# Kernel optimization log

Hardware: AMD Instinct MI355X
Metric: run time of the kernel (lower is better)

The kernel has to match this reference:

```python
import jax, jax.numpy as jnp
import numpy as np
import math

DIM = 147      # input feature dim
EMB = 64       # in_dim * head_cnt
M = 32         # int(EMB * kernel_ratio)
EPS_LN = 1e-5
EPS = 1e-8


def layer_norm(x, g, b, eps=EPS_LN):
    mu = jnp.mean(x, axis=-1, keepdims=True)
    var = jnp.mean(jnp.square(x - mu), axis=-1, keepdims=True)
    return (x - mu) * jax.lax.rsqrt(var + eps) * g + b


def prm_exp(x, W_rf):
    # x: [b, t, e], W_rf: [m, e]
    xd = 0.5 * jnp.sum(x * x, axis=-1, keepdims=True)        # [b, t, 1]
    wtx = jnp.einsum('bte,me->btm', x, W_rf)                  # [b, t, m]
    return jnp.exp(wtx - xd) / math.sqrt(M)


def setup_inputs() -> dict:
    key = jax.random.key(0)
    ks = jax.random.split(key, 16)
    B, T = 32, 3136
    s_in = 1.0 / math.sqrt(DIM)
    s_emb = 1.0 / math.sqrt(EMB)
    inp = {
        'x':      jax.random.normal(ks[0], (B, T, DIM), jnp.float32),
        'w_kqv':  jax.random.uniform(ks[1], (3 * EMB, DIM), jnp.float32, -s_in, s_in),
        'b_kqv':  jax.random.uniform(ks[2], (3 * EMB,), jnp.float32, -s_in, s_in),
        'w_proj': jax.random.uniform(ks[3], (EMB, EMB), jnp.float32, -s_emb, s_emb),
        'b_proj': jax.random.uniform(ks[4], (EMB,), jnp.float32, -s_emb, s_emb),
        'g1':     jnp.ones((DIM,), jnp.float32),
        'beta1':  jnp.zeros((DIM,), jnp.float32),
        'g2':     jnp.ones((EMB,), jnp.float32),
        'beta2':  jnp.zeros((EMB,), jnp.float32),
        'w_m1':   jax.random.uniform(ks[5], (EMB, EMB), jnp.float32, -s_emb, s_emb),
        'b_m1':   jax.random.uniform(ks[6], (EMB,), jnp.float32, -s_emb, s_emb),
        'w_m2':   jax.random.uniform(ks[7], (EMB, EMB), jnp.float32, -s_emb, s_emb),
        'b_m2':   jax.random.uniform(ks[8], (EMB,), jnp.float32, -s_emb, s_emb),
        # orthogonal random-feature matrix scaled by sqrt(m) (buffer 'w')
        'W_rf':   jnp.asarray(np.linalg.qr(np.random.RandomState(0).randn(EMB, EMB))[0][:M] * math.sqrt(M), jnp.float32),
    }
    return inp


def reference(x, w_kqv, b_kqv, w_proj, b_proj, g1, beta1, g2, beta2,
              w_m1, b_m1, w_m2, b_m2, W_rf):
    # --- single_attn(norm1(x)) ---
    xn = layer_norm(x, g1, beta1)
    kqv = xn @ w_kqv.T + b_kqv                                  # [b, t, 3e]
    k, q, v = jnp.split(kqv, 3, axis=-1)
    kp = prm_exp(k, W_rf)                                       # [b, t, m]
    qp = prm_exp(q, W_rf)                                       # [b, t, m]
    D = jnp.einsum('btm,bm->bt', qp, kp.sum(axis=1))[..., None]  # [b, t, 1]
    kptv = jnp.einsum('bte,btm->bem', v, kp)                    # [b, e, m]
    y = jnp.einsum('btm,bem->bte', qp, kptv) / (D + EPS)        # [b, t, e]
    y = v + (y @ w_proj.T + b_proj)                             # residual on v
    # --- y + mlp(norm2(y)) ---
    yn = layer_norm(y, g2, beta2)
    h = jax.nn.gelu(yn @ w_m1.T + b_m1, approximate=False)
    out = y + (h @ w_m2.T + b_m2)
    return out
```

## Files before the change

kernel.cpp:

```cpp
#include <hip/hip_runtime.h>
#include <hip/hip_bf16.h>

#define BB 32
#define TT 3136
#define DD 147
#define EE 64
#define MM 32
#define BT (BB*TT)

typedef __hip_bfloat16 bf16;
typedef __attribute__((ext_vector_type(8))) short s8v;
typedef __attribute__((ext_vector_type(4))) float f4v;

__device__ __forceinline__ float b2f(bf16 v){ return __bfloat162float(v); }
__device__ __forceinline__ bf16 f2b(float v){ return __float2bfloat16(v); }
__device__ __forceinline__ unsigned pack2(float a, float b){
  union { bf16 h[2]; unsigned u; } cv; cv.h[0]=f2b(a); cv.h[1]=f2b(b); return cv.u;
}

template<typename T>
__device__ __forceinline__ float cvt1(T v);
template<> __device__ __forceinline__ float cvt1<float>(float v){ return v; }
template<> __device__ __forceinline__ float cvt1<bf16>(bf16 v){ return __bfloat162float(v); }

__global__ void k_detect(const unsigned* __restrict__ g1u, int* __restrict__ flagp){
  if (threadIdx.x == 0 && blockIdx.x == 0)
    *flagp = (g1u[0] == 0x3F803F80u) ? 1 : 0;
}

template<typename T>
__device__ void cvt_body(int idx,
    const T* wkqv, const T* bkqv, const T* Wrf, const T* wproj, const T* bproj,
    const T* g2, const T* be2, const T* wm1, const T* bm1, const T* wm2,
    const T* bm2, const T* g1, const T* be1,
    bf16* Bprep, bf16* WrfB, bf16* w0B, float* bprojF,
    float* g2F, float* be2F, bf16* w1B, float* bm1F, bf16* w2B,
    float* bm2F, float* c2F)
{
  if (idx < 30720){
    int n = idx/160, k = idx - n*160;
    Bprep[idx] = f2b(k < DD ? cvt1(wkqv[n*DD + k]) * cvt1(g1[k]) : 0.f);
    return;
  }
  idx -= 30720;
  if (idx < 2048){ WrfB[idx] = f2b(cvt1(Wrf[idx])); return; }
  idx -= 2048;
  if (idx < 4608){
    int e = idx/72, c = idx - e*72;
    w0B[idx] = f2b(c < 64 ? cvt1(wproj[e*64 + c]) : 0.f); return;
  }
  idx -= 4608;
  if (idx < 64){ bprojF[idx] = cvt1(bproj[idx]); return; }
  idx -= 64;
  if (idx < 64){ g2F[idx] = cvt1(g2[idx]); return; }
  idx -= 64;
  if (idx < 64){ be2F[idx] = cvt1(be2[idx]); return; }
  idx -= 64;
  if (idx < 4608){
    int e = idx/72, c = idx - e*72;
    w1B[idx] = f2b(c < 64 ? cvt1(wm1[e*64 + c]) : 0.f); return;
  }
  idx -= 4608;
  if (idx < 64){ bm1F[idx] = cvt1(bm1[idx]); return; }
  idx -= 64;
  if (idx < 4608){
    int e = idx/72, c = idx - e*72;
    w2B[idx] = f2b(c < 64 ? cvt1(wm2[e*64 + c]) : 0.f); return;
  }
  idx -= 4608;
  if (idx < 64){ bm2F[idx] = cvt1(bm2[idx]); return; }
  idx -= 64;
  if (idx < 192){
    float s = cvt1(bkqv[idx]);
    for (int k=0; k<DD; ++k)
      s = fmaf(cvt1(wkqv[idx*DD + k]), cvt1(be1[k]), s);
    c2F[idx] = s; return;
  }
}

__global__ void k_cvt(const void* wkqv, const void* bkqv, const void* Wrf,
    const void* wproj, const void* bproj, const void* g2, const void* be2,
    const void* wm1, const void* bm1, const void* wm2, const void* bm2,
    const void* g1, const void* be1, const int* __restrict__ flagp,
    bf16* Bprep, bf16* WrfB, bf16* w0B, float* bprojF,
    float* g2F, float* be2F, bf16* w1B, float* bm1F, bf16* w2B,
    float* bm2F, float* c2F,
    float* __restrict__ kptvF, float* __restrict__ ksumF)
{
  int idx = blockIdx.x*256 + threadIdx.x;
  if (idx < 65536) kptvF[idx] = 0.f;
  if (idx < 1024)  ksumF[idx] = 0.f;
  if (*flagp)
    cvt_body<bf16>(idx, (const bf16*)wkqv, (const bf16*)bkqv, (const bf16*)Wrf,
      (const bf16*)wproj, (const bf16*)bproj, (const bf16*)g2, (const bf16*)be2,
      (const bf16*)wm1, (const bf16*)bm1, (const bf16*)wm2, (const bf16*)bm2,
      (const bf16*)g1, (const bf16*)be1,
      Bprep, WrfB, w0B, bprojF, g2F, be2F, w1B, bm1F, w2B, bm2F, c2F);
  else
    cvt_body<float>(idx, (const float*)wkqv, (const float*)bkqv, (const float*)Wrf,
      (const float*)wproj, (const float*)bproj, (const float*)g2, (const float*)be2,
      (const float*)wm1, (const float*)bm1, (const float*)wm2, (const float*)bm2,
      (const float*)g1, (const float*)be1,
      Bprep, WrfB, w0B, bprojF, g2F, be2F, w1B, bm1F, w2B, bm2F, c2F);
}

__global__ __launch_bounds__(256) void k_a2(
    const void* __restrict__ x, const int* __restrict__ flagp,
    const bf16* __restrict__ Bprep, const float* __restrict__ c2F,
    const bf16* __restrict__ WrfB,
    bf16* __restrict__ qp, bf16* __restrict__ v,
    float* __restrict__ kptvF, float* __restrict__ ksumF)
{
  __shared__ __align__(16) char smem[40320];
  bf16* xRaw = (bf16*)smem;
  bf16* aS   = (bf16*)(smem + 18816);
  bf16* vT   = (bf16*)(smem + 18816);
  bf16* kpT  = (bf16*)(smem + 18816 + 9216);

  int tid = threadIdx.x;
  size_t t0 = (size_t)blockIdx.x*64;
  int b = blockIdx.x / 49;

  int tw = tid>>6, lane = tid&63, quad = lane>>4, r = lane&15;
  int tRow = tw*16 + quad*4;

  if (*flagp){
    const uint4* xg = (const uint4*)((const bf16*)x + t0*DD);
    uint4* xo = (uint4*)xRaw;
    for (int c=tid; c<1176; c+=256) xo[c] = xg[c];
  } else {
    const float4* xg = (const float4*)((const float*)x + t0*DD);
    uint2* xo = (uint2*)xRaw;
    for (int c=tid; c<2352; c+=256){
      float4 f = xg[c];
      uint2 u; u.x = pack2(f.x, f.y); u.y = pack2(f.z, f.w);
      xo[c] = u;
    }
  }
  __syncthreads();

  int ti = lane>>2, s = lane&3;
  int row = tw*16 + ti;
  const bf16* srow = xRaw + row*DD;
  float s1 = 0.f, s2 = 0.f;
  #pragma unroll
  for (int j=0; j<37; ++j){
    int e = s + 4*j;
    if (e < DD){
      float vx = b2f(srow[e]);
      s1 += vx;
      s2 = fmaf(vx, vx, s2);
    }
  }
  s1 += __shfl_xor(s1,1); s1 += __shfl_xor(s1,2);
  s2 += __shfl_xor(s2,1); s2 += __shfl_xor(s2,2);
  float mu  = s1 * (1.f/147.f);
  float var = s2 * (1.f/147.f) - mu*mu;
  float rn  = rsqrtf(var + 1e-5f);

  bf16* arow = aS + row*168;
  #pragma unroll
  for (int j=0; j<37; ++j){
    int e = s + 4*j;
    arow[e] = (e < DD) ? f2b((b2f(srow[e]) - mu)*rn) : f2b(0.f);
  }
  arow[148+s] = f2b(0.f); arow[152+s] = f2b(0.f); arow[156+s] = f2b(0.f);

  f4v zero = {0.f,0.f,0.f,0.f};

  f4v acc[12];
  #pragma unroll
  for (int nt=0; nt<12; ++nt) acc[nt] = zero;
  const bf16* aBase = &aS[(tw*16+r)*168 + quad*8];
  const bf16* bBase = &Bprep[r*160 + quad*8];
  #pragma unroll 1
  for (int ks=0; ks<5; ++ks){
    s8v a = *((const s8v*)(aBase + ks*32));
    #pragma unroll
    for (int nt=0; nt<12; ++nt){
      s8v bw = *((const s8v*)(bBase + nt*16*160 + ks*32));
      acc[nt] = __builtin_amdgcn_mfma_f32_16x16x32_bf16(a, bw, acc[nt], 0,0,0);
    }
  }

  float c2v[12];
  #pragma unroll
  for (int nt=0; nt<12; ++nt) c2v[nt] = c2F[nt*16 + r];

  float vv[4][4];
  #pragma unroll
  for (int nt=8; nt<12; ++nt){
    #pragma unroll
    for (int reg=0; reg<4; ++reg){
      vv[nt-8][reg] = acc[nt][reg] + c2v[nt];
      v[(t0 + tRow + reg)*64 + (nt-8)*16 + r] = f2b(vv[nt-8][reg]);
    }
  }

  float kq[8][4];
  #pragma unroll
  for (int nt=0; nt<8; ++nt)
    #pragma unroll
    for (int reg=0; reg<4; ++reg)
      kq[nt][reg] = acc[nt][reg] + c2v[nt];

  bf16* kqW = (bf16*)(smem + tw*4704);
  #pragma unroll
  for (int nt=0; nt<8; ++nt)
    #pragma unroll
    for (int reg=0; reg<4; ++reg)
      kqW[(quad*4+reg)*136 + nt*16 + r] = f2b(kq[nt][reg]);

  float xdk[4], xdq[4];
  #pragma unroll
  for (int reg=0; reg<4; ++reg){
    float sk = 0.f, sq = 0.f;
    #pragma unroll
    for (int nt=0; nt<4; ++nt){
      sk = fmaf(kq[nt][reg],   kq[nt][reg],   sk);
      sq = fmaf(kq[nt+4][reg], kq[nt+4][reg], sq);
    }
    #pragma unroll
    for (int off=1; off<16; off<<=1){
      sk += __shfl_xor(sk, off);
      sq += __shfl_xor(sq, off);
    }
    xdk[reg] = 0.5f*sk;
    xdq[reg] = 0.5f*sq;
  }

  f4v accP[2] = {zero, zero}, accQ[2] = {zero, zero};
  #pragma unroll
  for (int ks=0; ks<2; ++ks){
    s8v ak = *((const s8v*)&kqW[r*136 + ks*32 + quad*8]);
    s8v aq = *((const s8v*)&kqW[r*136 + 64 + ks*32 + quad*8]);
    #pragma unroll
    for (int nt=0; nt<2; ++nt){
      s8v wf = *((const s8v*)&WrfB[(nt*16+r)*64 + ks*32 + quad*8]);
      accP[nt] = __builtin_amdgcn_mfma_f32_16x16x32_bf16(ak, wf, accP[nt], 0,0,0);
      accQ[nt] = __builtin_amdgcn_mfma_f32_16x16x32_bf16(aq, wf, accQ[nt], 0,0,0);
    }
  }
  float kpv[2][4];
  #pragma unroll
  for (int nt=0; nt<2; ++nt){
    #pragma unroll
    for (int reg=0; reg<4; ++reg){
      size_t gt = t0 + tRow + reg;
      kpv[nt][reg] = expf(accP[nt][reg] - xdk[reg]) * 0.17677669529663687f;
      qp[gt*32 + nt*16 + r] = f2b(expf(accQ[nt][reg] - xdq[reg]) * 0.17677669529663687f);
    }
  }
  __syncthreads();

  #pragma unroll
  for (int nt=0; nt<4; ++nt){
    *((unsigned*)&vT[(nt*16+r)*72 + tRow])     = pack2(vv[nt][0], vv[nt][1]);
    *((unsigned*)&vT[(nt*16+r)*72 + tRow + 2]) = pack2(vv[nt][2], vv[nt][3]);
  }
  #pragma unroll
  for (int nt=0; nt<2; ++nt){
    *((unsigned*)&kpT[(nt*16+r)*72 + tRow])     = pack2(kpv[nt][0], kpv[nt][1]);
    *((unsigned*)&kpT[(nt*16+r)*72 + tRow + 2]) = pack2(kpv[nt][2], kpv[nt][3]);
  }

  float ks0 = kpv[0][0]+kpv[0][1]+kpv[0][2]+kpv[0][3];
  float ks1 = kpv[1][0]+kpv[1][1]+kpv[1][2]+kpv[1][3];
  ks0 += __shfl_xor(ks0, 16); ks0 += __shfl_xor(ks0, 32);
  ks1 += __shfl_xor(ks1, 16); ks1 += __shfl_xor(ks1, 32);
  if (lane < 16){
    atomicAdd(&ksumF[b*32 + r],      ks0);
    atomicAdd(&ksumF[b*32 + 16 + r], ks1);
  }
  __syncthreads();

  f4v accKV[2] = {zero, zero};
  #pragma unroll
  for (int kh=0; kh<2; ++kh){
    s8v av = *((const s8v*)&vT[(tw*16+r)*72 + kh*32 + quad*8]);
    #pragma unroll
    for (int nt=0; nt<2; ++nt){
      s8v bk = *((const s8v*)&kpT[(nt*16+r)*72 + kh*32 + quad*8]);
      accKV[nt] = __builtin_amdgcn_mfma_f32_16x16x32_bf16(av, bk, accKV[nt], 0,0,0);
    }
  }
  float* dst = kptvF + b*2048;
  #pragma unroll
  for (int nt=0; nt<2; ++nt)
    #pragma unroll
    for (int reg=0; reg<4; ++reg)
      atomicAdd(&dst[(tw*16 + quad*4 + reg)*32 + nt*16 + r], accKV[nt][reg]);
}

__global__ __launch_bounds__(256,2) void k_b(
    const bf16* __restrict__ qp, const bf16* __restrict__ v,
    const float* __restrict__ kptvF, const float* __restrict__ ksumF,
    const bf16* __restrict__ w0B, const float* __restrict__ bprojF,
    const float* __restrict__ g2F, const float* __restrict__ be2F,
    const bf16* __restrict__ w1B, const float* __restrict__ bm1F,
    const bf16* __restrict__ w2B, const float* __restrict__ bm2F,
    const int* __restrict__ flagp, void* __restrict__ outp)
{
  __shared__ __align__(16) bf16 qpS[64*40];
  __shared__ __align__(16) bf16 kvS[64*40];
  __shared__ __align__(16) bf16 w0S[64*72];
  __shared__ __align__(16) bf16 w1S[64*72];
  __shared__ __align__(16) bf16 w2S[64*72];
  __shared__ __align__(16) bf16 vS[64*72];
  __shared__ __align__(16) bf16 stA[64*72];
  __shared__ __align__(16) bf16 stB[64*72];
  __shared__ float ksS[32];
  __shared__ float bpS[64], b1S[64], b2S[64], gS[64], btS[64];

  int flag = *flagp;
  int tid = threadIdx.x;
  int b = blockIdx.y;
  int gt0 = b*TT + blockIdx.x*64;

  {
    int t = tid>>2, q = tid&3;
    uint4 u = ((const uint4*)(qp + (size_t)gt0*32))[tid];
    *((uint4*)&qpS[t*40 + q*8]) = u;
  }
  for (int i=tid; i<512; i+=256){
    int e = i>>3, q = i&7;
    float4 f = ((const float4*)(kptvF + b*2048))[i];
    union { bf16 h[4]; uint2 u; } cv;
    cv.h[0]=f2b(f.x); cv.h[1]=f2b(f.y); cv.h[2]=f2b(f.z); cv.h[3]=f2b(f.w);
    *((uint2*)&kvS[e*40 + q*4]) = cv.u;
  }
  for (int i=tid; i<512; i+=256){
    int t = i>>3, q = i&7;
    uint4 u = ((const uint4*)(v + (size_t)gt0*64))[i];
    *((uint4*)&vS[t*72 + q*8]) = u;
  }
  for (int i=tid; i<576; i+=256) ((uint4*)w0S)[i] = ((const uint4*)w0B)[i];
  for (int i=tid; i<576; i+=256) ((uint4*)w1S)[i] = ((const uint4*)w1B)[i];
  for (int i=tid; i<576; i+=256) ((uint4*)w2S)[i] = ((const uint4*)w2B)[i];
  if (tid<32) ksS[tid] = ksumF[b*32+tid];
  if (tid<64){
    bpS[tid]=bprojF[tid]; b1S[tid]=bm1F[tid]; b2S[tid]=bm2F[tid];
    gS[tid]=g2F[tid]; btS[tid]=be2F[tid];
  }
  __syncthreads();

  int tw = tid>>6, lane = tid&63, quad = lane>>4, r = lane&15;
  int tRow = tw*16 + quad*4;
  f4v zero = {0.f,0.f,0.f,0.f};

  float dpart;
  {
    int ti = lane>>2, sl = lane&3;
    const bf16* qrow = &qpS[(tw*16+ti)*40];
    float s = 0.f;
    #pragma unroll
    for (int m=0; m<8; ++m) s = fmaf(b2f(qrow[sl*8+m]), ksS[sl*8+m], s);
    s += __shfl_xor(s,1); s += __shfl_xor(s,2);
    dpart = s;
  }
  float Dinv[4];
  #pragma unroll
  for (int reg=0; reg<4; ++reg){
    float d = __shfl(dpart, (lane & 0x30) + 4*reg);
    Dinv[reg] = 1.f/(d + 1e-8f);
  }

  f4v accA[4];
  {
    s8v aq = *((const s8v*)&qpS[(tw*16+r)*40 + quad*8]);
    #pragma unroll
    for (int nt=0; nt<4; ++nt){
      s8v bk = *((const s8v*)&kvS[(nt*16+r)*40 + quad*8]);
      accA[nt] = __builtin_amdgcn_mfma_f32_16x16x32_bf16(aq, bk, zero, 0,0,0);
    }
  }

  #pragma unroll
  for (int nt=0; nt<4; ++nt)
    #pragma unroll
    for (int reg=0; reg<4; ++reg)
      stA[(tRow+reg)*72 + nt*16 + r] = f2b(accA[nt][reg]*Dinv[reg]);

  f4v accY[4] = {zero, zero, zero, zero};
  #pragma unroll
  for (int kh=0; kh<2; ++kh){
    s8v ay = *((const s8v*)&stA[(tw*16+r)*72 + kh*32 + quad*8]);
    #pragma unroll
    for (int nt=0; nt<4; ++nt){
      s8v bw = *((const s8v*)&w0S[(nt*16+r)*72 + kh*32 + quad*8]);
      accY[nt] = __builtin_amdgcn_mfma_f32_16x16x32_bf16(ay, bw, accY[nt], 0,0,0);
    }
  }
  float y[4][4];
  #pragma unroll
  for (int nt=0; nt<4; ++nt){
    int e = nt*16 + r;
    float bp = bpS[e];
    #pragma unroll
    for (int reg=0; reg<4; ++reg)
      y[nt][reg] = accY[nt][reg] + b2f(vS[(tRow+reg)*72 + e]) + bp;
  }

  float mu[4], rs[4];
  #pragma unroll
  for (int reg=0; reg<4; ++reg){
    float s = y[0][reg]+y[1][reg]+y[2][reg]+y[3][reg];
    #pragma unroll
    for (int off=1; off<16; off<<=1) s += __shfl_xor(s, off);
    mu[reg] = s * (1.f/64.f);
  }
  #pragma unroll
  for (int reg=0; reg<4; ++reg){
    float d2 = 0.f;
    #pragma unroll
    for (int nt=0; nt<4; ++nt){ float d = y[nt][reg]-mu[reg]; d2 = fmaf(d,d,d2); }
    #pragma unroll
    for (int off=1; off<16; off<<=1) d2 += __shfl_xor(d2, off);
    rs[reg] = rsqrtf(d2*(1.f/64.f) + 1e-5f);
  }
  #pragma unroll
  for (int nt=0; nt<4; ++nt){
    int e = nt*16 + r;
    float g = gS[e], be = btS[e];
    #pragma unroll
    for (int reg=0; reg<4; ++reg)
      stB[(tRow+reg)*72 + e] = f2b((y[nt][reg]-mu[reg])*rs[reg]*g + be);
  }

  f4v accH[4] = {zero, zero, zero, zero};
  #pragma unroll
  for (int kh=0; kh<2; ++kh){
    s8v ah = *((const s8v*)&stB[(tw*16+r)*72 + kh*32 + quad*8]);
    #pragma unroll
    for (int nt=0; nt<4; ++nt){
      s8v bw = *((const s8v*)&w1S[(nt*16+r)*72 + kh*32 + quad*8]);
      accH[nt] = __builtin_amdgcn_mfma_f32_16x16x32_bf16(ah, bw, accH[nt], 0,0,0);
    }
  }
  #pragma unroll
  for (int nt=0; nt<4; ++nt){
    int e = nt*16 + r;
    float b1 = b1S[e];
    #pragma unroll
    for (int reg=0; reg<4; ++reg){
      float h = accH[nt][reg] + b1;
      h = 0.5f*h*(1.f + erff(h*0.70710678118654752f));
      stA[(tRow+reg)*72 + e] = f2b(h);
    }
  }

  f4v accO[4] = {zero, zero, zero, zero};
  #pragma unroll
  for (int kh=0; kh<2; ++kh){
    s8v ao = *((const s8v*)&stA[(tw*16+r)*72 + kh*32 + quad*8]);
    #pragma unroll
    for (int nt=0; nt<4; ++nt){
      s8v bw = *((const s8v*)&w2S[(nt*16+r)*72 + kh*32 + quad*8]);
      accO[nt] = __builtin_amdgcn_mfma_f32_16x16x32_bf16(ao, bw, accO[nt], 0,0,0);
    }
  }
  if (flag){
    bf16* o = (bf16*)outp;
    #pragma unroll
    for (int nt=0; nt<4; ++nt){
      int e = nt*16 + r;
      float b2 = b2S[e];
      #pragma unroll
      for (int reg=0; reg<4; ++reg)
        o[(size_t)(gt0 + tRow + reg)*64 + e] = f2b(y[nt][reg] + accO[nt][reg] + b2);
    }
  } else {
    float* o = (float*)outp;
    #pragma unroll
    for (int nt=0; nt<4; ++nt){
      int e = nt*16 + r;
      float b2 = b2S[e];
      #pragma unroll
      for (int reg=0; reg<4; ++reg)
        o[(size_t)(gt0 + tRow + reg)*64 + e] = y[nt][reg] + accO[nt][reg] + b2;
    }
  }
}

extern "C" void kernel_launch(void* const* d_in, const int* in_sizes, int n_in,
                              void* d_out, int out_size, void* d_ws, size_t ws_size,
                              hipStream_t stream){
  const void* x    = d_in[0];
  const void* wkqv = d_in[1];
  const void* bkqv = d_in[2];
  const void* wproj= d_in[3];
  const void* bproj= d_in[4];
  const void* g1   = d_in[5];
  const void* be1  = d_in[6];
  const void* g2   = d_in[7];
  const void* be2  = d_in[8];
  const void* wm1  = d_in[9];
  const void* bm1  = d_in[10];
  const void* wm2  = d_in[11];
  const void* bm2  = d_in[12];
  const void* Wrf  = d_in[13];

  char* ws = (char*)d_ws;
  int*   flagp = (int*)(ws + 0);
  bf16*  Bprep = (bf16*) (ws + 256);
  bf16*  WrfB  = (bf16*) (ws + 62464);
  bf16*  w0B   = (bf16*) (ws + 66560);
  float* bprojF= (float*)(ws + 82944);
  float* g2F   = (float*)(ws + 83200);
  float* be2F  = (float*)(ws + 83456);
  bf16*  w1B   = (bf16*) (ws + 83712);
  float* bm1F  = (float*)(ws + 100096);
  bf16*  w2B   = (bf16*) (ws + 100352);
  float* bm2F  = (float*)(ws + 116736);
  float* c2F   = (float*)(ws + 118784);
  float* kptvF = (float*)(ws + 32231424);
  float* ksumF = (float*)(ws + 32493568);
  bf16*  qp    = (bf16*) (ws + 32497664);
  bf16*  v     = (bf16*) (ws + 38920192);

  k_detect<<<1, 64, 0, stream>>>((const unsigned*)g1, flagp);
  k_cvt<<<256, 256, 0, stream>>>(wkqv, bkqv, Wrf, wproj, bproj, g2, be2,
      wm1, bm1, wm2, bm2, g1, be1, flagp,
      Bprep, WrfB, w0B, bprojF, g2F, be2F, w1B, bm1F, w2B, bm2F,
      c2F, kptvF, ksumF);
  k_a2<<<BT/64, 256, 0, stream>>>(x, flagp, Bprep, c2F, WrfB,
      qp, v, kptvF, ksumF);
  k_b<<<dim3(TT/64, BB), 256, 0, stream>>>(qp, v, kptvF, ksumF,
      w0B, bprojF, g2F, be2F, w1B, bm1F, w2B, bm2F, flagp, d_out);
}
```

Baseline: 204.0 us.

## Use per-wave LDS strips in k_a2, drop detect kernel, raise occupancy

```diff
diff --git a/kernel.cpp b/kernel.cpp
--- a/kernel.cpp
+++ b/kernel.cpp
@@ -23,9 +23,8 @@
 template<> __device__ __forceinline__ float cvt1<float>(float v){ return v; }
 template<> __device__ __forceinline__ float cvt1<bf16>(bf16 v){ return __bfloat162float(v); }
 
-__global__ void k_detect(const unsigned* __restrict__ g1u, int* __restrict__ flagp){
-  if (threadIdx.x == 0 && blockIdx.x == 0)
-    *flagp = (g1u[0] == 0x3F803F80u) ? 1 : 0;
+__device__ __forceinline__ int bf16flag(const void* g1){
+  return (*(const unsigned*)g1 == 0x3F803F80u) ? 1 : 0;
 }
 
 template<typename T>
@@ -81,7 +80,7 @@
 __global__ void k_cvt(const void* wkqv, const void* bkqv, const void* Wrf,
     const void* wproj, const void* bproj, const void* g2, const void* be2,
     const void* wm1, const void* bm1, const void* wm2, const void* bm2,
-    const void* g1, const void* be1, const int* __restrict__ flagp,
+    const void* g1, const void* be1,
     bf16* Bprep, bf16* WrfB, bf16* w0B, float* bprojF,
     float* g2F, float* be2F, bf16* w1B, float* bm1F, bf16* w2B,
     float* bm2F, float* c2F,
@@ -90,7 +89,7 @@
   int idx = blockIdx.x*256 + threadIdx.x;
   if (idx < 65536) kptvF[idx] = 0.f;
   if (idx < 1024)  ksumF[idx] = 0.f;
-  if (*flagp)
+  if (bf16flag(g1))
     cvt_body<bf16>(idx, (const bf16*)wkqv, (const bf16*)bkqv, (const bf16*)Wrf,
       (const bf16*)wproj, (const bf16*)bproj, (const bf16*)g2, (const bf16*)be2,
       (const bf16*)wm1, (const bf16*)bm1, (const bf16*)wm2, (const bf16*)bm2,
@@ -104,18 +103,16 @@
       Bprep, WrfB, w0B, bprojF, g2F, be2F, w1B, bm1F, w2B, bm2F, c2F);
 }
 
-__global__ __launch_bounds__(256) void k_a2(
-    const void* __restrict__ x, const int* __restrict__ flagp,
+__global__ __launch_bounds__(256,4) void k_a2(
+    const void* __restrict__ x, const void* __restrict__ g1,
     const bf16* __restrict__ Bprep, const float* __restrict__ c2F,
     const bf16* __restrict__ WrfB,
     bf16* __restrict__ qp, bf16* __restrict__ v,
     float* __restrict__ kptvF, float* __restrict__ ksumF)
 {
-  __shared__ __align__(16) char smem[40320];
-  bf16* xRaw = (bf16*)smem;
-  bf16* aS   = (bf16*)(smem + 18816);
-  bf16* vT   = (bf16*)(smem + 18816);
-  bf16* kpT  = (bf16*)(smem + 18816 + 9216);
+  __shared__ __align__(16) char smem[21504];
+  bf16* vT   = (bf16*)smem;
+  bf16* kpT  = (bf16*)(smem + 9216);
 
   int tid = threadIdx.x;
   size_t t0 = (size_t)blockIdx.x*64;
@@ -123,34 +120,44 @@
 
   int tw = tid>>6, lane = tid&63, quad = lane>>4, r = lane&15;
   int tRow = tw*16 + quad*4;
-
-  if (*flagp){
-    const uint4* xg = (const uint4*)((const bf16*)x + t0*DD);
-    uint4* xo = (uint4*)xRaw;
-    for (int c=tid; c<1176; c+=256) xo[c] = xg[c];
+  char* strip = smem + tw*5376;
+  bf16* lin = (bf16*)strip;
+  bf16* aS  = (bf16*)strip;
+  bf16* kqW = (bf16*)strip;
+
+  if (bf16flag(g1)){
+    const uint4* xg = (const uint4*)((const bf16*)x + (t0 + (size_t)tw*16)*DD);
+    uint4* xo = (uint4*)lin;
+    #pragma unroll
+    for (int k=0; k<5; ++k){
+      int c = k*64 + lane;
+      if (c < 294) xo[c] = xg[c];
+    }
   } else {
-    const float4* xg = (const float4*)((const float*)x + t0*DD);
-    uint2* xo = (uint2*)xRaw;
-    for (int c=tid; c<2352; c+=256){
-      float4 f = xg[c];
-      uint2 u; u.x = pack2(f.x, f.y); u.y = pack2(f.z, f.w);
-      xo[c] = u;
-    }
-  }
-  __syncthreads();
-
-  int ti = lane>>2, s = lane&3;
-  int row = tw*16 + ti;
-  const bf16* srow = xRaw + row*DD;
+    const float4* xg = (const float4*)((const float*)x + (t0 + (size_t)tw*16)*DD);
+    uint2* xo = (uint2*)lin;
+    #pragma unroll
+    for (int k=0; k<10; ++k){
+      int c = k*64 + lane;
+      if (c < 588){
+        float4 f = xg[c];
+        uint2 u; u.x = pack2(f.x, f.y); u.y = pack2(f.z, f.w);
+        xo[c] = u;
+      }
+    }
+  }
+
+  int ti = lane>>2, sl = lane&3;
+  const bf16* srow = lin + ti*DD;
+  float xv[37];
   float s1 = 0.f, s2 = 0.f;
   #pragma unroll
   for (int j=0; j<37; ++j){
-    int e = s + 4*j;
-    if (e < DD){
-      float vx = b2f(srow[e]);
-      s1 += vx;
-      s2 = fmaf(vx, vx, s2);
-    }
+    int e = sl + 4*j;
+    float vx = (e < DD) ? b2f(srow[e]) : 0.f;
+    xv[j] = vx;
+    s1 += vx;
+    s2 = fmaf(vx, vx, s2);
   }
   s1 += __shfl_xor(s1,1); s1 += __shfl_xor(s1,2);
   s2 += __shfl_xor(s2,1); s2 += __shfl_xor(s2,2);
@@ -158,20 +165,21 @@
   float var = s2 * (1.f/147.f) - mu*mu;
   float rn  = rsqrtf(var + 1e-5f);
 
-  bf16* arow = aS + row*168;
+  bf16* arow = aS + ti*168;
   #pragma unroll
   for (int j=0; j<37; ++j){
-    int e = s + 4*j;
-    arow[e] = (e < DD) ? f2b((b2f(srow[e]) - mu)*rn) : f2b(0.f);
-  }
-  arow[148+s] = f2b(0.f); arow[152+s] = f2b(0.f); arow[156+s] = f2b(0.f);
+    int e = sl + 4*j;
+    if (e < DD)       arow[e] = f2b((xv[j]-mu)*rn);
+    else if (e == DD) arow[e] = f2b(0.f);
+  }
+  arow[148+sl] = f2b(0.f); arow[152+sl] = f2b(0.f); arow[156+sl] = f2b(0.f);
 
   f4v zero = {0.f,0.f,0.f,0.f};
 
   f4v acc[12];
   #pragma unroll
   for (int nt=0; nt<12; ++nt) acc[nt] = zero;
-  const bf16* aBase = &aS[(tw*16+r)*168 + quad*8];
+  const bf16* aBase = aS + r*168 + quad*8;
   const bf16* bBase = &Bprep[r*160 + quad*8];
   #pragma unroll 1
   for (int ks=0; ks<5; ++ks){
@@ -204,7 +212,6 @@
     for (int reg=0; reg<4; ++reg)
       kq[nt][reg] = acc[nt][reg] + c2v[nt];
 
-  bf16* kqW = (bf16*)(smem + tw*4704);
   #pragma unroll
   for (int nt=0; nt<8; ++nt)
     #pragma unroll
@@ -299,7 +306,7 @@
     const float* __restrict__ g2F, const float* __restrict__ be2F,
     const bf16* __restrict__ w1B, const float* __restrict__ bm1F,
     const bf16* __restrict__ w2B, const float* __restrict__ bm2F,
-    const int* __restrict__ flagp, void* __restrict__ outp)
+    const void* __restrict__ g1, void* __restrict__ outp)
 {
   __shared__ __align__(16) bf16 qpS[64*40];
   __shared__ __align__(16) bf16 kvS[64*40];
@@ -312,7 +319,7 @@
   __shared__ float ksS[32];
   __shared__ float bpS[64], b1S[64], b2S[64], gS[64], btS[64];
 
-  int flag = *flagp;
+  int flag = bf16flag(g1);
   int tid = threadIdx.x;
   int b = blockIdx.y;
   int gt0 = b*TT + blockIdx.x*64;
@@ -501,7 +508,6 @@
   const void* Wrf  = d_in[13];
 
   char* ws = (char*)d_ws;
-  int*   flagp = (int*)(ws + 0);
   bf16*  Bprep = (bf16*) (ws + 256);
   bf16*  WrfB  = (bf16*) (ws + 62464);
   bf16*  w0B   = (bf16*) (ws + 66560);
@@ -518,13 +524,12 @@
   bf16*  qp    = (bf16*) (ws + 32497664);
   bf16*  v     = (bf16*) (ws + 38920192);
 
-  k_detect<<<1, 64, 0, stream>>>((const unsigned*)g1, flagp);
   k_cvt<<<256, 256, 0, stream>>>(wkqv, bkqv, Wrf, wproj, bproj, g2, be2,
-      wm1, bm1, wm2, bm2, g1, be1, flagp,
+      wm1, bm1, wm2, bm2, g1, be1,
       Bprep, WrfB, w0B, bprojF, g2F, be2F, w1B, bm1F, w2B, bm2F,
       c2F, kptvF, ksumF);
-  k_a2<<<BT/64, 256, 0, stream>>>(x, flagp, Bprep, c2F, WrfB,
+  k_a2<<<BT/64, 256, 0, stream>>>(x, g1, Bprep, c2F, WrfB,
       qp, v, kptvF, ksumF);
   k_b<<<dim3(TT/64, BB), 256, 0, stream>>>(qp, v, kptvF, ksumF,
-      w0B, bprojF, g2F, be2F, w1B, bm1F, w2B, bm2F, flagp, d_out);
-}
+      w0B, bprojF, g2F, be2F, w1B, bm1F, w2B, bm2F, g1, d_out);
+}
```

Result: faster. 199.7 us (-2.1%).
